# Performance work log

Measured on AMD Instinct MI355X. Metric: run time of the kernel, lower is better.

## Reference

```python
import jax, jax.numpy as jnp
import numpy as np
from functools import partial

FRAME_RATE = 100
MIN_BPM = 55.0
MAX_BPM = 215.0
THRESHOLD = 0.05
TRANSITION_LAMBDA = 100.0  # madmom-style exponential tempo-change penalty
NEG = jnp.float32(-1e9)


def _build_dbn():
    """Bar-pointer DBN: one block of `tau` phase states per tempo interval tau."""
    min_int = int(round(60.0 * FRAME_RATE / MAX_BPM))
    max_int = int(round(60.0 * FRAME_RATE / MIN_BPM))
    intervals = np.arange(min_int, max_int + 1)              # (T_tempi,)
    state_positions = np.concatenate([np.arange(t) for t in intervals])  # (S,)
    first_idx = np.cumsum(intervals) - intervals             # pos-0 state per tempo
    last_idx = np.cumsum(intervals) - 1                      # last state per tempo
    # exponential tempo-transition distribution, row-normalized in log space
    ratio = intervals[None, :].astype(np.float64) / intervals[:, None]
    raw = -TRANSITION_LAMBDA * np.abs(ratio - 1.0)
    trans_log = raw - np.log(np.exp(raw - raw.max(1, keepdims=True)).sum(1, keepdims=True)) - raw.max(1, keepdims=True)
    return (
        jnp.asarray(state_positions == 0),                    # pos0_mask (S,) bool
        jnp.asarray(first_idx, dtype=jnp.int32),
        jnp.asarray(last_idx, dtype=jnp.int32),
        jnp.asarray(trans_log, dtype=jnp.float32),            # (T_tempi, T_tempi)
    )


def setup_inputs() -> dict:
    key = jax.random.key(0)
    logit = jax.random.normal(key, (4, 6000), dtype=jnp.float32)
    return {"logit": logit}


@jax.jit
def reference(logit):
    pos0_mask, first_idx, last_idx, trans_log = _build_dbn()
    S = pos0_mask.shape[0]
    B, T = logit.shape

    beat_lp = jax.nn.log_sigmoid(logit)      # (B, T)
    nonbeat_lp = jax.nn.log_sigmoid(-logit)  # (B, T)

    def emission(b_t, nb_t):
        # (B, S): beat log-prob on phase-0 states, non-beat elsewhere
        return jnp.where(pos0_mask[None, :], b_t[:, None], nb_t[:, None])

    # ---- Viterbi forward pass with backpointers ----
    def step(delta, xs):
        b_t, nb_t = xs
        prev_last = delta[:, last_idx]                         # (B, T_tempi)
        cand = prev_last[:, :, None] + trans_log[None, :, :]   # (B, from, to)
        from_beat = cand.max(axis=1)                           # (B, T_tempi)
        bp_beat = last_idx[cand.argmax(axis=1)]                # (B, T_tempi)
        # within-tempo advance: state s comes from s-1 (blocks are contiguous)
        shifted = jnp.concatenate(
            [jnp.full((B, 1), NEG, delta.dtype), delta[:, :-1]], axis=1)
        combined = shifted.at[:, first_idx].set(from_beat)
        new_delta = combined + emission(b_t, nb_t)
        bp = jnp.broadcast_to(jnp.arange(S, dtype=jnp.int32) - 1, (B, S))
        bp = bp.at[:, first_idx].set(bp_beat)
        return new_delta, bp

    delta0 = emission(beat_lp[:, 0], nonbeat_lp[:, 0]) - jnp.log(jnp.float32(S))
    xs = (beat_lp[:, 1:].T, nonbeat_lp[:, 1:].T)               # each (T-1, B)
    delta_final, bps = jax.lax.scan(step, delta0, xs)          # bps: (T-1, B, S)

    # ---- backtrack ----
    final_state = jnp.argmax(delta_final, axis=1).astype(jnp.int32)  # (B,)

    def back(state, bp_t):
        prev = jnp.take_along_axis(bp_t, state[:, None], axis=1)[:, 0]
        return prev, state

    state0, ys = jax.lax.scan(back, final_state, bps, reverse=True)
    path = jnp.concatenate([state0[None, :], ys], axis=0)      # (T, B) state ids

    on_beat = pos0_mask[path].T                                # (B, T)
    act = jax.nn.sigmoid(logit)
    beat_mask = on_beat & (act >= jnp.float32(THRESHOLD))
    return beat_mask.astype(jnp.float32)                       # 1.0 at beat frames
```

## Files before the change

### kernel.cpp

```cpp
#include <hip/hip_runtime.h>
#include <math.h>

#define NTAU 82
#define TMIN 28
#define S_TOT 5617
#define TF 6000
#define BATCH 4
#define WMAX 28
#define AP 84
#define NTHREADS 1024
#define NCHUNK 215
#define CHUNK_F (WMAX * AP)
#define NPOS 41
#define FLAG_STRIDE 64

#define TRANS_OFF 0
#define BLP_OFF   8192
#define NBLP_OFF  32768
#define AH_OFF    57344
#define FLAG_OFF  (AH_OFF + BATCH * NCHUNK * CHUNK_F)
#define RESV_OFF  (FLAG_OFF + 8 * FLAG_STRIDE)
#define RESI_OFF  (RESV_OFF + 8)

typedef float v2f __attribute__((ext_vector_type(2)));

__device__ __forceinline__ int first_of(int b) { return b * (55 + b) / 2; }

__device__ __forceinline__ float logsig(float x) {
    return -(fmaxf(-x, 0.0f) + log1pf(expf(-fabsf(x))));
}

__global__ void k_trans(float* __restrict__ ws) {
    int i = blockIdx.x;
    int j = threadIdx.x;
    __shared__ double sh[128];
    double raw = 0.0, e = 0.0;
    double ti = 28.0 + (double)i;
    if (j < NTAU) {
        double tj = 28.0 + (double)j;
        raw = -100.0 * fabs(tj / ti - 1.0);
        e = exp(raw);
    }
    sh[j] = e;
    __syncthreads();
    for (int st = 64; st > 0; st >>= 1) {
        if (j < st) sh[j] += sh[j + st];
        __syncthreads();
    }
    double lse = log(sh[0]);
    if (j < NTAU) ws[TRANS_OFF + i * NTAU + j] = (float)(raw - lse);
}

__global__ void k_emis(const float* __restrict__ logit, float* __restrict__ ws,
                       float* __restrict__ out) {
    int idx = blockIdx.x * blockDim.x + threadIdx.x;
    if (idx < BATCH * TF) {
        float x = logit[idx];
        ws[BLP_OFF + idx]  = logsig(x);
        ws[NBLP_OFF + idx] = logsig(-x);
        out[idx] = 0.0f;
    }
}

__global__ void k_flags(int* __restrict__ flags) {
    int i = blockIdx.x * blockDim.x + threadIdx.x;
    if (i < 8 * FLAG_STRIDE) flags[i] = 0;
}

__global__ __attribute__((amdgpu_flat_work_group_size(NTHREADS, NTHREADS),
                          amdgpu_waves_per_eu(4, 4),
                          amdgpu_num_vgpr(128)))
void k_viterbi(const float* __restrict__ logit,
               const float* __restrict__ transg,
               const float* __restrict__ blp_all,
               const float* __restrict__ nblp_all,
               float* __restrict__ Ah_all,
               int*   __restrict__ flags,
               float* __restrict__ resv,
               int*   __restrict__ resi,
               float* __restrict__ out) {
    const int tid = threadIdx.x;
    const int b   = blockIdx.x >> 1;
    const int h   = blockIdx.x & 1;

    const float* blp  = blp_all  + b * TF;
    const float* nblp = nblp_all + b * TF;
    float* Ah = Ah_all + (size_t)b * (NCHUNK * CHUNK_F);
    int* flagOut = flags + (b * 2 + h) * FLAG_STRIDE;
    int* flagIn  = flags + (b * 2 + (1 - h)) * FLAG_STRIDE;

    __shared__ float V[2832];
    __shared__ __align__(16) float A_lds[CHUNK_F];
    __shared__ __align__(16) float fb[CHUNK_F];
    __shared__ __align__(16) float win_nb[4][WMAX];
    __shared__ __align__(16) float win_b[4][WMAX];
    __shared__ float wv[16];
    __shared__ int   wi[16];
    __shared__ int   sstate;

    const int iseg = tid & 3;
    const int jpp  = (tid >> 2) % 21;
    const int tg   = tid / 84;
    const bool p2act = (tid < 1008);
    const int i0 = iseg * 20;
    const int j0 = 4 * jpp + h;
    const bool j1v = (jpp < 20);
    const int j1 = j1v ? (4 * jpp + 2 + h) : j0;

    float tr0[22], tr1[22];
#pragma unroll
    for (int k = 0; k < 22; ++k) { tr0[k] = -1.0e30f; tr1[k] = -1.0e30f; }
    if (p2act) {
        const int icnt = (iseg == 3) ? 22 : 20;
#pragma unroll
        for (int k = 0; k < 22; ++k) {
            if (k < icnt) {
                tr0[k] = transg[(i0 + k) * NTAU + j0];
                if (j1v) tr1[k] = transg[(i0 + k) * NTAU + j1];
            }
        }
    }

    const bool ract = (tid < 1008);
    const int ro = ract ? (tid / 36) : 27;
    const int sp = tid % 36;
    const bool rv2 = ract && (sp < 5);
    const int pA = sp, pB = sp + 36;
    const int colA = 2 * pA + h, colB = 2 * pB + h;
    const int tauA = 28 + 2 * pA + h, tauB = 28 + 2 * pB + h;
    const int foA = pA * (27 + pA + h), foB = pB * (27 + pB + h);
    int rrA = ro, rrB = ro;

    const int NF_TOT = NPOS * (NPOS - 1 + h);
    int nrR[2], nrFo[2], nrTau[2];
    bool nrV[2];
#pragma unroll
    for (int q = 0; q < 2; ++q) {
        const int f = tid + q * NTHREADS;
        nrV[q] = (f < NF_TOT);
        nrR[q] = 28; nrFo[q] = 0; nrTau[q] = 109;
        if (nrV[q]) {
            int lo = 0, hi = NPOS - 1;
            while (lo < hi) { int mid = (lo + hi + 1) >> 1;
                              if (mid * (mid - 1 + h) <= f) lo = mid; else hi = mid - 1; }
            const int m = f - lo * (lo - 1 + h);
            nrR[q]   = TMIN + m;
            nrFo[q]  = lo * (27 + lo + h);
            nrTau[q] = TMIN + 2 * lo + h;
        }
    }

    const int ttI0 = tid / 41, psI0 = tid % 41;
    const int offI0 = ttI0 * AP + 2 * psI0 + (1 - h);
    const bool vI1 = (tid < 124);
    const int ttI1 = (tid + 1024) / 41, psI1 = (tid + 1024) % 41;
    const int offI1 = ttI1 * AP + 2 * psI1 + (1 - h);

    const float logS = (float)log((double)S_TOT);
    const float b0 = blp[0], n0 = nblp[0];
    const int SOWN = NPOS * (68 + h);
    for (int g = tid; g < SOWN; g += NTHREADS) {
        int lo = 0, hi = NPOS - 1;
        while (lo < hi) { int mid = (lo + hi + 1) >> 1;
                          if (mid * (27 + mid + h) <= g) lo = mid; else hi = mid - 1; }
        const int tau = TMIN + 2 * lo + h;
        const int r = g - lo * (27 + lo + h);
        V[g] = ((r == tau - 1) ? b0 : n0) - logS;
    }

    auto winload = [&](int cc) {
        if (cc < NCHUNK && tid < WMAX) {
            int gt = 1 + cc * WMAX + tid;
            win_nb[cc & 3][tid] = (gt < TF) ? nblp[gt] : 0.0f;
            win_b [cc & 3][tid] = (gt < TF) ? blp[gt]  : 0.0f;
        }
    };
    winload(0);
    winload(1);
    __syncthreads();

#define PH2_STEP2(av, aw, ka, kb) { \
    float x0 = (av) + tr0[ka]; float y0 = (aw) + tr0[kb]; \
    m0 = fmaxf(fmaxf(m0, x0), y0); \
    float x1 = (av) + tr1[ka]; float y1 = (aw) + tr1[kb]; \
    m1 = fmaxf(fmaxf(m1, x1), y1); }

    float cvA = 0.0f, cvB = 0.0f;
    for (int c = 0; c < NCHUNK; ++c) {
        const int buf = c & 3;
        float* AhC = Ah + (size_t)c * CHUNK_F;

        float nbr[WMAX];
        {
            const float4* wn4 = (const float4*)&win_nb[buf][0];
#pragma unroll
            for (int qq = 0; qq < 7; ++qq) {
                float4 t4 = wn4[qq];
                nbr[4*qq+0] = t4.x; nbr[4*qq+1] = t4.y; nbr[4*qq+2] = t4.z; nbr[4*qq+3] = t4.w;
            }
        }

        cvA = ract ? V[foA + rrA] : 0.0f;
        cvB = rv2  ? V[foB + rrB] : 0.0f;
        for (int tt = 0; tt < ro; ++tt) {
            const float w = win_nb[buf][tt];
            cvA += w; cvB += w;
        }
        if (ract) {
            A_lds[ro * AP + colA] = cvA;
            __hip_atomic_store(&AhC[ro * AP + colA], cvA,
                               __ATOMIC_RELAXED, __HIP_MEMORY_SCOPE_AGENT);
            if (rv2) {
                A_lds[ro * AP + colB] = cvB;
                __hip_atomic_store(&AhC[ro * AP + colB], cvB,
                                   __ATOMIC_RELAXED, __HIP_MEMORY_SCOPE_AGENT);
            }
        }
        winload(c + 2);
        __syncthreads();

        if (tid == 0)
            __hip_atomic_store(flagOut, c + 1, __ATOMIC_RELAXED, __HIP_MEMORY_SCOPE_AGENT);

        {
            const int a0 = nrFo[0] + nrR[0];
            const int a1 = nrV[1] ? (nrFo[1] + nrR[1]) : a0;
            v2f v01 = v2f{V[a0], V[a1]};
#pragma unroll
            for (int tt = 0; tt < WMAX; ++tt) v01 += v2f{nbr[tt], nbr[tt]};
            V[a0] = v01.x;
            if (nrV[1]) V[a1] = v01.y;
        }

        if (tid == 0) {
            int guard = 0;
            while (__hip_atomic_load(flagIn, __ATOMIC_RELAXED, __HIP_MEMORY_SCOPE_AGENT) < c + 1) {
                __builtin_amdgcn_s_sleep(1);
                if (++guard > (1 << 24)) break;
            }
        }
        __syncthreads();

        A_lds[offI0] = __hip_atomic_load(&AhC[offI0],
                                         __ATOMIC_RELAXED, __HIP_MEMORY_SCOPE_AGENT);
        if (vI1)
            A_lds[offI1] = __hip_atomic_load(&AhC[offI1],
                                             __ATOMIC_RELAXED, __HIP_MEMORY_SCOPE_AGENT);
        __syncthreads();

        if (p2act) {
#pragma unroll
            for (int u = 0; u < 3; ++u) {
                const int tl = tg + 12 * u;
                if (tl < WMAX) {
                    const float4* ar4 = (const float4*)&A_lds[tl * AP + i0];
                    const float4 a0 = ar4[0], a1 = ar4[1], a2 = ar4[2],
                                 a3 = ar4[3], a4 = ar4[4];
                    float m0 = -INFINITY, m1 = -INFINITY;
                    PH2_STEP2(a0.x, a0.y, 0, 1)   PH2_STEP2(a0.z, a0.w, 2, 3)
                    PH2_STEP2(a1.x, a1.y, 4, 5)   PH2_STEP2(a1.z, a1.w, 6, 7)
                    PH2_STEP2(a2.x, a2.y, 8, 9)   PH2_STEP2(a2.z, a2.w, 10, 11)
                    PH2_STEP2(a3.x, a3.y, 12, 13) PH2_STEP2(a3.z, a3.w, 14, 15)
                    PH2_STEP2(a4.x, a4.y, 16, 17) PH2_STEP2(a4.z, a4.w, 18, 19)
                    if (iseg == 3) {
                        float a20 = A_lds[tl * AP + 80];
                        float a21 = A_lds[tl * AP + 81];
                        PH2_STEP2(a20, a21, 20, 21)
                    }
                    m0 = fmaxf(m0, __shfl_xor(m0, 1)); m1 = fmaxf(m1, __shfl_xor(m1, 1));
                    m0 = fmaxf(m0, __shfl_xor(m0, 2)); m1 = fmaxf(m1, __shfl_xor(m1, 2));
                    if (iseg == 0) {
                        fb[tl * AP + j0] = m0;
                        if (j1v) fb[tl * AP + j1] = m1;
                    }
                }
            }
        }
        __syncthreads();

        {
            const float bw = win_b[buf][ro];
            float eA = ract ? (fb[ro * AP + colA] + bw) : 0.0f;
            float eB = rv2  ? (fb[ro * AP + colB] + bw) : 0.0f;
            for (int tt = ro + 1; tt < WMAX; ++tt) {
                const float w = win_nb[buf][tt];
                eA += w; eB += w;
            }
            const bool keepC = (c == NCHUNK - 1) && (ro >= 7);
            if (ract) {
                V[foA + rrA] = keepC ? cvA : eA;
                if (rv2) V[foB + rrB] = keepC ? cvB : eB;
            }
            rrA += WMAX; if (rrA >= tauA) rrA -= tauA;
            rrB += WMAX; if (rrB >= tauB) rrB -= tauB;
        }
#pragma unroll
        for (int q = 0; q < 2; ++q) {
            if (nrV[q]) { nrR[q] += WMAX; if (nrR[q] >= nrTau[q]) nrR[q] -= nrTau[q]; }
        }
        __syncthreads();
    }
#undef PH2_STEP2

    float bvv = -INFINITY; int bss = 0x7fffffff;
    for (int g = tid; g < SOWN; g += NTHREADS) {
        int lo = 0, hi = NPOS - 1;
        while (lo < hi) { int mid = (lo + hi + 1) >> 1;
                          if (mid * (27 + mid + h) <= g) lo = mid; else hi = mid - 1; }
        const int tau = TMIN + 2 * lo + h;
        const int r = g - lo * (27 + lo + h);
        const int p = (5998 - r) % tau;
        const int s = first_of(2 * lo + h) + p;
        const float v = V[g];
        if (v > bvv || (v == bvv && s < bss)) { bvv = v; bss = s; }
    }
#pragma unroll
    for (int d = 1; d < 64; d <<= 1) {
        float ov = __shfl_xor(bvv, d);
        int   os = __shfl_xor(bss, d);
        if (ov > bvv || (ov == bvv && os < bss)) { bvv = ov; bss = os; }
    }
    if ((tid & 63) == 0) { wv[tid >> 6] = bvv; wi[tid >> 6] = bss; }
    __syncthreads();

    if (tid == 0) {
        float bv = wv[0]; int bs = wi[0];
#pragma unroll
        for (int k = 1; k < 16; ++k) {
            if (wv[k] > bv || (wv[k] == bv && wi[k] < bs)) { bv = wv[k]; bs = wi[k]; }
        }
        resv[b * 2 + h] = bv;
        resi[b * 2 + h] = bs;
        __hip_atomic_fetch_add(flagOut, 1, __ATOMIC_RELEASE, __HIP_MEMORY_SCOPE_AGENT);
        wv[0] = bv; wi[0] = bs;
    }
    if (h == 1) return;
    __syncthreads();

    if (tid == 0) {
        int guard = 0;
        while (__hip_atomic_load(flagIn, __ATOMIC_RELAXED, __HIP_MEMORY_SCOPE_AGENT) < NCHUNK + 1) {
            __builtin_amdgcn_s_sleep(1);
            if (++guard > (1 << 26)) break;
        }
        int fv = __hip_atomic_load(flagIn, __ATOMIC_ACQUIRE, __HIP_MEMORY_SCOPE_AGENT);
        if (fv == -0x7fffffff) wv[1] = -1.0e30f;
        float bv = wv[0]; int bs = wi[0];
        const float pv = resv[b * 2 + 1];
        const int   ps = resi[b * 2 + 1];
        if (pv > bv || (pv == bv && ps < bs)) { bv = pv; bs = ps; }
        sstate = bs;
    }
    __syncthreads();

    if (tid < 64) {
        const int lane = tid;
        int s = sstate;
        int t = TF - 1;
        for (int guard = 0; guard < 400; ++guard) {
            int lo = 0, hi = NTAU - 1;
            while (lo < hi) { int mid = (lo + hi + 1) >> 1;
                              if (first_of(mid) <= s) lo = mid; else hi = mid - 1; }
            int j = lo;
            int p = s - first_of(j);
            int tb = t - p;
            if (tb < 0) break;
            if (lane == 0) {
                float x = logit[b * TF + tb];
                float act = 1.0f / (1.0f + expf(-x));
                if (act >= 0.05f) out[b * TF + tb] = 1.0f;
            }
            if (tb == 0) break;
            const int tq = tb - 1;
            const float* arow = Ah + (size_t)(tq / WMAX) * CHUNK_F + (tq % WMAX) * AP;
            float cvv = arow[lane] + transg[lane * NTAU + j];
            int ci = lane;
            if (lane < NTAU - 64) {
                float c2 = arow[64 + lane] + transg[(64 + lane) * NTAU + j];
                if (c2 > cvv) { cvv = c2; ci = 64 + lane; }
            }
#pragma unroll
            for (int d = 1; d < 64; d <<= 1) {
                float ov = __shfl_xor(cvv, d, 64);
                int   oi = __shfl_xor(ci, d, 64);
                if (ov > cvv || (ov == cvv && oi < ci)) { cvv = ov; ci = oi; }
            }
            s = first_of(ci) + (TMIN + ci) - 1;
            t = tb - 1;
        }
    }
}

extern "C" void kernel_launch(void* const* d_in, const int* in_sizes, int n_in,
                              void* d_out, int out_size, void* d_ws, size_t ws_size,
                              hipStream_t stream) {
    const float* logit = (const float*)d_in[0];
    float* out = (float*)d_out;
    float* ws = (float*)d_ws;
    k_trans<<<dim3(NTAU), dim3(128), 0, stream>>>(ws);
    k_emis<<<dim3((BATCH * TF + 255) / 256), dim3(256), 0, stream>>>(logit, ws, out);
    k_flags<<<dim3(2), dim3(256), 0, stream>>>((int*)(ws + FLAG_OFF));
    k_viterbi<<<dim3(BATCH * 2), dim3(NTHREADS), 0, stream>>>(
        logit, ws + TRANS_OFF, ws + BLP_OFF, ws + NBLP_OFF, ws + AH_OFF,
        (int*)(ws + FLAG_OFF), ws + RESV_OFF, (int*)(ws + RESI_OFF), out);
}
```

Baseline: 1.303 ms.

## Split Ah by parity to overlap own-half max with peer exchange

Stores the per-chunk beat-transition row values split by tempo parity, so each workgroup's own half sits contiguously in both LDS and global memory. Each block now computes the max over its own half before waiting on the peer's half, overlapping that work with the cross-block exchange. The peer half is copied with float4 loads instead of scalar atomic loads. This adds a padding-init kernel and makes the backtrack use an interleaved index mapping, and the peer data is now read with plain vector loads rather than atomic loads.

After: 1.246 ms (median of 2 runs). 1.05x faster.

```diff
diff --git a/kernel.cpp b/kernel.cpp
--- a/kernel.cpp
+++ b/kernel.cpp
@@ -8,9 +8,11 @@
 #define BATCH 4
 #define WMAX 28
 #define AP 84
+#define LP 96
+#define GP 88
 #define NTHREADS 1024
 #define NCHUNK 215
-#define CHUNK_F (WMAX * AP)
+#define CHUNK_G (WMAX * GP)
 #define NPOS 41
 #define FLAG_STRIDE 64
 
@@ -18,7 +20,7 @@
 #define BLP_OFF   8192
 #define NBLP_OFF  32768
 #define AH_OFF    57344
-#define FLAG_OFF  (AH_OFF + BATCH * NCHUNK * CHUNK_F)
+#define FLAG_OFF  (AH_OFF + BATCH * NCHUNK * CHUNK_G)
 #define RESV_OFF  (FLAG_OFF + 8 * FLAG_STRIDE)
 #define RESI_OFF  (RESV_OFF + 8)
 
@@ -65,6 +67,19 @@
 __global__ void k_flags(int* __restrict__ flags) {
     int i = blockIdx.x * blockDim.x + threadIdx.x;
     if (i < 8 * FLAG_STRIDE) flags[i] = 0;
+}
+
+__global__ void k_ahpad(float* __restrict__ Ah) {
+    int i = blockIdx.x * blockDim.x + threadIdx.x;
+    const int total = BATCH * NCHUNK * WMAX * 2 * 3;
+    if (i < total) {
+        int c3 = i % 3; int rest = i / 3;
+        int par = rest & 1; rest >>= 1;
+        int row = rest % WMAX; rest /= WMAX;
+        int chunk = rest % NCHUNK; int bb = rest / NCHUNK;
+        Ah[(size_t)bb * NCHUNK * CHUNK_G + (size_t)chunk * CHUNK_G
+           + row * GP + par * 44 + 41 + c3] = -1.0e30f;
+    }
 }
 
 __global__ __attribute__((amdgpu_flat_work_group_size(NTHREADS, NTHREADS),
@@ -85,13 +100,13 @@
 
     const float* blp  = blp_all  + b * TF;
     const float* nblp = nblp_all + b * TF;
-    float* Ah = Ah_all + (size_t)b * (NCHUNK * CHUNK_F);
+    float* Ah = Ah_all + (size_t)b * (NCHUNK * CHUNK_G);
     int* flagOut = flags + (b * 2 + h) * FLAG_STRIDE;
     int* flagIn  = flags + (b * 2 + (1 - h)) * FLAG_STRIDE;
 
     __shared__ float V[2832];
-    __shared__ __align__(16) float A_lds[CHUNK_F];
-    __shared__ __align__(16) float fb[CHUNK_F];
+    __shared__ __align__(16) float A_lds[WMAX * LP];
+    __shared__ __align__(16) float fb[CHUNK_G];
     __shared__ __align__(16) float win_nb[4][WMAX];
     __shared__ __align__(16) float win_b[4][WMAX];
     __shared__ float wv[16];
@@ -102,21 +117,29 @@
     const int jpp  = (tid >> 2) % 21;
     const int tg   = tid / 84;
     const bool p2act = (tid < 1008);
-    const int i0 = iseg * 20;
+    const int p0s = iseg * 12;
     const int j0 = 4 * jpp + h;
     const bool j1v = (jpp < 20);
     const int j1 = j1v ? (4 * jpp + 2 + h) : j0;
 
-    float tr0[22], tr1[22];
-#pragma unroll
-    for (int k = 0; k < 22; ++k) { tr0[k] = -1.0e30f; tr1[k] = -1.0e30f; }
+    float trO0[12], trO1[12], trP0[12], trP1[12];
+#pragma unroll
+    for (int k = 0; k < 12; ++k) {
+        trO0[k] = -1.0e30f; trO1[k] = -1.0e30f;
+        trP0[k] = -1.0e30f; trP1[k] = -1.0e30f;
+    }
     if (p2act) {
-        const int icnt = (iseg == 3) ? 22 : 20;
-#pragma unroll
-        for (int k = 0; k < 22; ++k) {
-            if (k < icnt) {
-                tr0[k] = transg[(i0 + k) * NTAU + j0];
-                if (j1v) tr1[k] = transg[(i0 + k) * NTAU + j1];
+#pragma unroll
+        for (int k = 0; k < 12; ++k) {
+            const int p = p0s + k;
+            if (p <= 40) {
+                const int iO = 2 * p + h, iP = 2 * p + 1 - h;
+                trO0[k] = transg[iO * NTAU + j0];
+                trP0[k] = transg[iP * NTAU + j0];
+                if (j1v) {
+                    trO1[k] = transg[iO * NTAU + j1];
+                    trP1[k] = transg[iP * NTAU + j1];
+                }
             }
         }
     }
@@ -126,7 +149,6 @@
     const int sp = tid % 36;
     const bool rv2 = ract && (sp < 5);
     const int pA = sp, pB = sp + 36;
-    const int colA = 2 * pA + h, colB = 2 * pB + h;
     const int tauA = 28 + 2 * pA + h, tauB = 28 + 2 * pB + h;
     const int foA = pA * (27 + pA + h), foB = pB * (27 + pB + h);
     int rrA = ro, rrB = ro;
@@ -150,12 +172,6 @@
         }
     }
 
-    const int ttI0 = tid / 41, psI0 = tid % 41;
-    const int offI0 = ttI0 * AP + 2 * psI0 + (1 - h);
-    const bool vI1 = (tid < 124);
-    const int ttI1 = (tid + 1024) / 41, psI1 = (tid + 1024) % 41;
-    const int offI1 = ttI1 * AP + 2 * psI1 + (1 - h);
-
     const float logS = (float)log((double)S_TOT);
     const float b0 = blp[0], n0 = nblp[0];
     const int SOWN = NPOS * (68 + h);
@@ -168,6 +184,8 @@
         V[g] = ((r == tau - 1) ? b0 : n0) - logS;
     }
 
+    for (int idx = tid; idx < WMAX * LP; idx += NTHREADS) A_lds[idx] = -1.0e30f;
+
     auto winload = [&](int cc) {
         if (cc < NCHUNK && tid < WMAX) {
             int gt = 1 + cc * WMAX + tid;
@@ -179,26 +197,17 @@
     winload(1);
     __syncthreads();
 
-#define PH2_STEP2(av, aw, ka, kb) { \
-    float x0 = (av) + tr0[ka]; float y0 = (aw) + tr0[kb]; \
+#define PH2P(av, aw, t0a, t0b, t1a, t1b) { \
+    float x0 = (av) + (t0a); float y0 = (aw) + (t0b); \
     m0 = fmaxf(fmaxf(m0, x0), y0); \
-    float x1 = (av) + tr1[ka]; float y1 = (aw) + tr1[kb]; \
+    float x1 = (av) + (t1a); float y1 = (aw) + (t1b); \
     m1 = fmaxf(fmaxf(m1, x1), y1); }
 
     float cvA = 0.0f, cvB = 0.0f;
+    float pm0[3], pm1[3];
     for (int c = 0; c < NCHUNK; ++c) {
         const int buf = c & 3;
-        float* AhC = Ah + (size_t)c * CHUNK_F;
-
-        float nbr[WMAX];
-        {
-            const float4* wn4 = (const float4*)&win_nb[buf][0];
-#pragma unroll
-            for (int qq = 0; qq < 7; ++qq) {
-                float4 t4 = wn4[qq];
-                nbr[4*qq+0] = t4.x; nbr[4*qq+1] = t4.y; nbr[4*qq+2] = t4.z; nbr[4*qq+3] = t4.w;
-            }
-        }
+        float* AhC = Ah + (size_t)c * CHUNK_G;
 
         cvA = ract ? V[foA + rrA] : 0.0f;
         cvB = rv2  ? V[foB + rrB] : 0.0f;
@@ -207,12 +216,12 @@
             cvA += w; cvB += w;
         }
         if (ract) {
-            A_lds[ro * AP + colA] = cvA;
-            __hip_atomic_store(&AhC[ro * AP + colA], cvA,
+            A_lds[ro * LP + h * 48 + pA] = cvA;
+            __hip_atomic_store(&AhC[ro * GP + h * 44 + pA], cvA,
                                __ATOMIC_RELAXED, __HIP_MEMORY_SCOPE_AGENT);
             if (rv2) {
-                A_lds[ro * AP + colB] = cvB;
-                __hip_atomic_store(&AhC[ro * AP + colB], cvB,
+                A_lds[ro * LP + h * 48 + pB] = cvB;
+                __hip_atomic_store(&AhC[ro * GP + h * 44 + pB], cvB,
                                    __ATOMIC_RELAXED, __HIP_MEMORY_SCOPE_AGENT);
             }
         }
@@ -221,13 +230,35 @@
 
         if (tid == 0)
             __hip_atomic_store(flagOut, c + 1, __ATOMIC_RELAXED, __HIP_MEMORY_SCOPE_AGENT);
+
+        if (p2act) {
+#pragma unroll
+            for (int u = 0; u < 3; ++u) {
+                const int tl = tg + 12 * u;
+                float m0 = -INFINITY, m1 = -INFINITY;
+                if (tl < WMAX) {
+                    const float4* ar4 = (const float4*)&A_lds[tl * LP + h * 48 + p0s];
+                    const float4 a0 = ar4[0], a1 = ar4[1], a2 = ar4[2];
+                    PH2P(a0.x, a0.y, trO0[0], trO0[1], trO1[0], trO1[1])
+                    PH2P(a0.z, a0.w, trO0[2], trO0[3], trO1[2], trO1[3])
+                    PH2P(a1.x, a1.y, trO0[4], trO0[5], trO1[4], trO1[5])
+                    PH2P(a1.z, a1.w, trO0[6], trO0[7], trO1[6], trO1[7])
+                    PH2P(a2.x, a2.y, trO0[8], trO0[9], trO1[8], trO1[9])
+                    PH2P(a2.z, a2.w, trO0[10], trO0[11], trO1[10], trO1[11])
+                }
+                pm0[u] = m0; pm1[u] = m1;
+            }
+        }
 
         {
             const int a0 = nrFo[0] + nrR[0];
             const int a1 = nrV[1] ? (nrFo[1] + nrR[1]) : a0;
             v2f v01 = v2f{V[a0], V[a1]};
 #pragma unroll
-            for (int tt = 0; tt < WMAX; ++tt) v01 += v2f{nbr[tt], nbr[tt]};
+            for (int tt = 0; tt < WMAX; ++tt) {
+                const float w = win_nb[buf][tt];
+                v01 += v2f{w, w};
+            }
             V[a0] = v01.x;
             if (nrV[1]) V[a1] = v01.y;
         }
@@ -241,11 +272,11 @@
         }
         __syncthreads();
 
-        A_lds[offI0] = __hip_atomic_load(&AhC[offI0],
-                                         __ATOMIC_RELAXED, __HIP_MEMORY_SCOPE_AGENT);
-        if (vI1)
-            A_lds[offI1] = __hip_atomic_load(&AhC[offI1],
-                                             __ATOMIC_RELAXED, __HIP_MEMORY_SCOPE_AGENT);
+        if (tid < 308) {
+            const int row = tid / 11, s4 = tid % 11;
+            const float4 v4 = *(const float4*)&AhC[row * GP + (1 - h) * 44 + s4 * 4];
+            *(float4*)&A_lds[row * LP + (1 - h) * 48 + s4 * 4] = v4;
+        }
         __syncthreads();
 
         if (p2act) {
@@ -253,20 +284,15 @@
             for (int u = 0; u < 3; ++u) {
                 const int tl = tg + 12 * u;
                 if (tl < WMAX) {
-                    const float4* ar4 = (const float4*)&A_lds[tl * AP + i0];
-                    const float4 a0 = ar4[0], a1 = ar4[1], a2 = ar4[2],
-                                 a3 = ar4[3], a4 = ar4[4];
-                    float m0 = -INFINITY, m1 = -INFINITY;
-                    PH2_STEP2(a0.x, a0.y, 0, 1)   PH2_STEP2(a0.z, a0.w, 2, 3)
-                    PH2_STEP2(a1.x, a1.y, 4, 5)   PH2_STEP2(a1.z, a1.w, 6, 7)
-                    PH2_STEP2(a2.x, a2.y, 8, 9)   PH2_STEP2(a2.z, a2.w, 10, 11)
-                    PH2_STEP2(a3.x, a3.y, 12, 13) PH2_STEP2(a3.z, a3.w, 14, 15)
-                    PH2_STEP2(a4.x, a4.y, 16, 17) PH2_STEP2(a4.z, a4.w, 18, 19)
-                    if (iseg == 3) {
-                        float a20 = A_lds[tl * AP + 80];
-                        float a21 = A_lds[tl * AP + 81];
-                        PH2_STEP2(a20, a21, 20, 21)
-                    }
+                    const float4* ar4 = (const float4*)&A_lds[tl * LP + (1 - h) * 48 + p0s];
+                    const float4 a0 = ar4[0], a1 = ar4[1], a2 = ar4[2];
+                    float m0 = pm0[u], m1 = pm1[u];
+                    PH2P(a0.x, a0.y, trP0[0], trP0[1], trP1[0], trP1[1])
+                    PH2P(a0.z, a0.w, trP0[2], trP0[3], trP1[2], trP1[3])
+                    PH2P(a1.x, a1.y, trP0[4], trP0[5], trP1[4], trP1[5])
+                    PH2P(a1.z, a1.w, trP0[6], trP0[7], trP1[6], trP1[7])
+                    PH2P(a2.x, a2.y, trP0[8], trP0[9], trP1[8], trP1[9])
+                    PH2P(a2.z, a2.w, trP0[10], trP0[11], trP1[10], trP1[11])
                     m0 = fmaxf(m0, __shfl_xor(m0, 1)); m1 = fmaxf(m1, __shfl_xor(m1, 1));
                     m0 = fmaxf(m0, __shfl_xor(m0, 2)); m1 = fmaxf(m1, __shfl_xor(m1, 2));
                     if (iseg == 0) {
@@ -279,6 +305,7 @@
         __syncthreads();
 
         {
+            const int colA = 2 * pA + h, colB = 2 * pB + h;
             const float bw = win_b[buf][ro];
             float eA = ract ? (fb[ro * AP + colA] + bw) : 0.0f;
             float eB = rv2  ? (fb[ro * AP + colB] + bw) : 0.0f;
@@ -300,7 +327,7 @@
         }
         __syncthreads();
     }
-#undef PH2_STEP2
+#undef PH2P
 
     float bvv = -INFINITY; int bss = 0x7fffffff;
     for (int g = tid; g < SOWN; g += NTHREADS) {
@@ -372,12 +399,13 @@
             }
             if (tb == 0) break;
             const int tq = tb - 1;
-            const float* arow = Ah + (size_t)(tq / WMAX) * CHUNK_F + (tq % WMAX) * AP;
-            float cvv = arow[lane] + transg[lane * NTAU + j];
+            const float* arow = Ah + (size_t)(tq / WMAX) * CHUNK_G + (tq % WMAX) * GP;
+            float cvv = arow[(lane & 1) * 44 + (lane >> 1)] + transg[lane * NTAU + j];
             int ci = lane;
             if (lane < NTAU - 64) {
-                float c2 = arow[64 + lane] + transg[(64 + lane) * NTAU + j];
-                if (c2 > cvv) { cvv = c2; ci = 64 + lane; }
+                const int i2 = 64 + lane;
+                float c2 = arow[(i2 & 1) * 44 + (i2 >> 1)] + transg[i2 * NTAU + j];
+                if (c2 > cvv) { cvv = c2; ci = i2; }
             }
 #pragma unroll
             for (int d = 1; d < 64; d <<= 1) {
@@ -400,6 +428,7 @@
     k_trans<<<dim3(NTAU), dim3(128), 0, stream>>>(ws);
     k_emis<<<dim3((BATCH * TF + 255) / 256), dim3(256), 0, stream>>>(logit, ws, out);
     k_flags<<<dim3(2), dim3(256), 0, stream>>>((int*)(ws + FLAG_OFF));
+    k_ahpad<<<dim3((BATCH * NCHUNK * WMAX * 2 * 3 + 255) / 256), dim3(256), 0, stream>>>(ws + AH_OFF);
     k_viterbi<<<dim3(BATCH * 2), dim3(NTHREADS), 0, stream>>>(
         logit, ws + TRANS_OFF, ws + BLP_OFF, ws + NBLP_OFF, ws + AH_OFF,
         (int*)(ws + FLAG_OFF), ws + RESV_OFF, (int*)(ws + RESI_OFF), out);
```
